# Optimization experiments

Hardware: AMD Instinct MI355X
Metric: run time of the kernel (lower is better)

## Reference

```python
import jax, jax.numpy as jnp
import numpy as np

EPS = 1e-5

def _layernorm(x, gamma, beta):
    mu = jnp.mean(x, axis=-1, keepdims=True)
    var = jnp.mean(jnp.square(x - mu), axis=-1, keepdims=True)
    return (x - mu) * jax.lax.rsqrt(var + EPS) * gamma + beta

def setup_inputs() -> dict:
    key = jax.random.key(0)
    k1, k2, k3 = jax.random.split(key, 3)
    T, B, D, H = 512, 32, 1024, 1024
    s_x = 1.0 / np.sqrt(D)
    s_h = 1.0 / np.sqrt(H)
    return {
        "input": jax.random.normal(k1, (T, B, D), dtype=jnp.float32),
        "h0": jnp.zeros((B, H), dtype=jnp.float32),
        "c0": jnp.zeros((B, H), dtype=jnp.float32),
        "Wx": jax.random.normal(k2, (4 * H, D), dtype=jnp.float32) * s_x,
        "Wh": jax.random.normal(k3, (4 * H, H), dtype=jnp.float32) * s_h,
        "gn_gamma": jnp.ones((4 * H,), dtype=jnp.float32),
        "gn_beta": jnp.zeros((4 * H,), dtype=jnp.float32),
        "cn_gamma": jnp.ones((H,), dtype=jnp.float32),
        "cn_beta": jnp.zeros((H,), dtype=jnp.float32),
    }

def reference(input, h0, c0, Wx, Wh, gn_gamma, gn_beta, cn_gamma, cn_beta):
    H = h0.shape[-1]
    # Precompute input projection for all timesteps: [T, B, 4H]
    gated_input = jnp.einsum('tbd,gd->tbg', input, Wx)

    def step(carry, gates_x):
        h, c = carry
        gates = gates_x + h @ Wh.T            # [B, 4H]
        gates = _layernorm(gates, gn_gamma, gn_beta)
        i, f, g, o = jnp.split(gates, 4, axis=1)
        c = jax.nn.sigmoid(f) * c + jax.nn.sigmoid(i) * jnp.tanh(g)
        c = _layernorm(c, cn_gamma, cn_beta)
        h = jax.nn.sigmoid(o) * jnp.tanh(c)
        return (h, c), h

    (h, c), output = jax.lax.scan(step, (h0, c0), gated_input)
    return output, h, c
```

## Files before the change

kernel.cpp:

```cpp
#include <hip/hip_runtime.h>
#include <hip/hip_bf16.h>

typedef __hip_bfloat16 bf16;
typedef __attribute__((ext_vector_type(4))) float f32x4;
typedef __attribute__((ext_vector_type(8))) short bf16x8;
typedef unsigned long long u64;
typedef unsigned short u16;
typedef unsigned u32;

#define T_STEPS 512
#define BATCH   32
#define DIM     1024
#define HID     1024
#define GATES   4096
#define NPROD   64
#define NOWN    32
#define NSCAN   (NPROD + NOWN)
#define MTILES  128
#define NTILES  16
#define NGEMM   (MTILES * NTILES)
#define MAGIC   0x5EED0001u

static __device__ __forceinline__ float sigmf(float x) {
    return 1.0f / (1.0f + __expf(-x));
}
static __device__ __forceinline__ float tanhfast(float x) {
    return 1.0f - 2.0f / (__expf(2.0f * x) + 1.0f);
}

static __device__ __forceinline__ u64 ldc_u64(const u64* p) {
    return __hip_atomic_load((u64*)p, __ATOMIC_RELAXED, __HIP_MEMORY_SCOPE_AGENT);
}
static __device__ __forceinline__ void stc_u64(u64* p, u64 v) {
    __hip_atomic_store(p, v, __ATOMIC_RELAXED, __HIP_MEMORY_SCOPE_AGENT);
}
static __device__ __forceinline__ void stc_u32(u32* p, u32 v) {
    __hip_atomic_store(p, v, __ATOMIC_RELAXED, __HIP_MEMORY_SCOPE_AGENT);
}
static __device__ __forceinline__ u32 ldc_u32(const u32* p) {
    return __hip_atomic_load((u32*)p, __ATOMIC_RELAXED, __HIP_MEMORY_SCOPE_AGENT);
}

static __device__ __forceinline__ bf16x8 cvt8(const float* p) {
    float4 x = *(const float4*)p;
    float4 y = *(const float4*)(p + 4);
    bf16x8 r;
    ((u16*)&r)[0] = __bfloat16_as_ushort(__float2bfloat16(x.x));
    ((u16*)&r)[1] = __bfloat16_as_ushort(__float2bfloat16(x.y));
    ((u16*)&r)[2] = __bfloat16_as_ushort(__float2bfloat16(x.z));
    ((u16*)&r)[3] = __bfloat16_as_ushort(__float2bfloat16(x.w));
    ((u16*)&r)[4] = __bfloat16_as_ushort(__float2bfloat16(y.x));
    ((u16*)&r)[5] = __bfloat16_as_ushort(__float2bfloat16(y.y));
    ((u16*)&r)[6] = __bfloat16_as_ushort(__float2bfloat16(y.z));
    ((u16*)&r)[7] = __bfloat16_as_ushort(__float2bfloat16(y.w));
    return r;
}

__global__ void init_kernel(u32* __restrict__ hx,
                            u64* __restrict__ gates_u,
                            u32* __restrict__ gxsent) {
    const size_t stride = (size_t)gridDim.x * blockDim.x;
    const size_t t0 = (size_t)blockIdx.x * blockDim.x + threadIdx.x;
    for (size_t i = t0; i < (size_t)BATCH * HID; i += stride) hx[i] = 0xFFFFFFFFu;
    for (size_t i = t0; i < (size_t)BATCH * GATES; i += stride) gates_u[i] = 0;
    for (size_t i = t0; i < (size_t)MTILES * NTILES; i += stride) gxsent[i] = 0u;
}

__global__ __launch_bounds__(512, 2) void fused_kernel(
    const float* __restrict__ input,
    const float* __restrict__ Wx,
    const float* __restrict__ Wh,
    const float* __restrict__ h0,
    const float* __restrict__ c0,
    const float* __restrict__ gn_g, const float* __restrict__ gn_b,
    const float* __restrict__ cn_g, const float* __restrict__ cn_b,
    u32* __restrict__ hx,
    u64* __restrict__ gates_u,
    bf16* __restrict__ gxT,
    u32* __restrict__ gxsent,
    float* __restrict__ out,
    float* __restrict__ h_final,
    float* __restrict__ c_final) {

    const int tid  = threadIdx.x;
    const int lane = tid & 63;
    const int w    = tid >> 6;

    if (blockIdx.x >= NSCAN) {
        const int gid = blockIdx.x - NSCAN;
        const int bm = gid >> 4;
        const int bn = gid & 15;
        const int wm = (w >> 2) * 64, wn = (w & 3) * 64;
        const int lr = lane & 15;
        const int ko = (lane >> 4) * 8;

        const float* Af = input + (size_t)(bm * 128 + wm + lr) * DIM + ko;
        const float* Bf = Wx    + (size_t)(bn * 256 + wn + lr) * DIM + ko;

        f32x4 acc[4][4] = {};
        for (int k = 0; k < DIM; k += 32) {
            bf16x8 af[4], bw[4];
#pragma unroll
            for (int m = 0; m < 4; ++m)
                af[m] = cvt8(Af + (size_t)m * 16 * DIM + k);
#pragma unroll
            for (int n = 0; n < 4; ++n)
                bw[n] = cvt8(Bf + (size_t)n * 16 * DIM + k);
#pragma unroll
            for (int m = 0; m < 4; ++m)
#pragma unroll
                for (int n = 0; n < 4; ++n)
                    acc[m][n] = __builtin_amdgcn_mfma_f32_16x16x32_bf16(af[m], bw[n], acc[m][n], 0, 0, 0);
        }
        const int cr = (lane >> 4) * 4;
        u64* gxT64 = (u64*)gxT;
#pragma unroll
        for (int m = 0; m < 4; ++m)
#pragma unroll
            for (int n = 0; n < 4; ++n) {
                int col = bn * 256 + wn + n * 16 + lr;
                int rb  = bm * 128 + wm + m * 16 + cr;
                u64 pk = 0;
#pragma unroll
                for (int r = 0; r < 4; ++r)
                    pk |= (u64)__bfloat16_as_ushort(__float2bfloat16(acc[m][n][r])) << (16 * r);
                stc_u64(gxT64 + (size_t)col * 4096 + (rb >> 2), pk);
            }
        asm volatile("s_waitcnt vmcnt(0)" ::: "memory");
        __syncthreads();
        if (tid == 0) stc_u32(gxsent + bm * NTILES + bn, MAGIC);
        return;
    }

    if (blockIdx.x < NPROD) {
        const int mi   = blockIdx.x & 1;
        const int g    = blockIdx.x >> 1;
        const int ni   = g * 8 + w;
        const int lr   = lane & 15;
        const int hi   = lane >> 4;
        const int ko   = hi * 8;
        const int cr   = hi * 4;
        const int gcol = ni * 16 + lr;
        const int brow = mi * 16 + cr;

        __shared__ __align__(16) char hsm[16 * 2048];

        const float* wf = Wh + (size_t)gcol * DIM + ko;
        bf16x8 bfrag[32];
#pragma unroll
        for (int kk = 0; kk < 32; ++kk)
            bfrag[kk] = cvt8(wf + kk * 32);

        const int arow = lr * 2048;
        const int axor = (lr & 7) << 4;

        const u64* gxT64 = (const u64*)gxT;
        const int ntile = g >> 1;
        u16 gxu[4];
        {
            int mtile = (2 * 0 + mi) >> 3;
            u32 sv = ldc_u32(gxsent + mtile * NTILES + ntile);
            while (sv != MAGIC) {
                __builtin_amdgcn_s_sleep(2);
                sv = ldc_u32(gxsent + mtile * NTILES + ntile);
            }
            u64 v = ldc_u64(gxT64 + (size_t)gcol * 4096 + 0 * 8 + mi * 4 + hi);
            gxu[0] = (u16)v; gxu[1] = (u16)(v >> 16);
            gxu[2] = (u16)(v >> 32); gxu[3] = (u16)(v >> 48);
        }

        for (int t = 0; t < T_STEPS; ++t) {
            {
                const int row0 = 2 * w + (lane >> 5);
                const int l5 = lane & 31;
                const u64* hsrc = (const u64*)(hx + (size_t)(mi * 16 + row0) * HID);
                char* drow = hsm + row0 * 2048;
                const int sx = (row0 & 7) << 4;
                const u32 want = (u32)t;
                u64 vv[16];
#pragma unroll
                for (int k = 0; k < 16; ++k)
                    vv[k] = ldc_u64(hsrc + k * 32 + l5);
                for (;;) {
                    bool ok = true;
#pragma unroll
                    for (int k = 0; k < 16; ++k) {
                        if ((((u32)(vv[k] >> 16) & 0xFFFFu) != want) ||
                            ((u32)(vv[k] >> 48) != want)) {
                            ok = false;
                            vv[k] = ldc_u64(hsrc + k * 32 + l5);
                        }
                    }
                    if (ok) break;
                    __builtin_amdgcn_s_sleep(1);
                }
#pragma unroll
                for (int k = 0; k < 16; ++k) {
                    int j = k * 32 + l5;
                    u32 packed = (u32)(vv[k] & 0xFFFFu) |
                                 (((u32)(vv[k] >> 32) & 0xFFFFu) << 16);
                    *(u32*)(drow + ((4 * j) ^ sx)) = packed;
                }
            }
            __syncthreads();

            {
                f32x4 acc = {0.f, 0.f, 0.f, 0.f};
#pragma unroll
                for (int kk = 0; kk < 32; ++kk) {
                    bf16x8 a = *(const bf16x8*)(hsm + arow + ((kk * 64 + ko * 2) ^ axor));
                    acc = __builtin_amdgcn_mfma_f32_16x16x32_bf16(a, bfrag[kk], acc, 0, 0, 0);
                }
                u64* gp = gates_u + (size_t)brow * GATES + gcol;
                const u64 tagup = (u64)(u32)(t + 1) << 32;
#pragma unroll
                for (int r = 0; r < 4; ++r) {
                    union { u16 u; bf16 h; } cv; cv.u = gxu[r];
                    float val = acc[r] + __bfloat162float(cv.h);
                    stc_u64(gp + (size_t)r * GATES, tagup | (u64)__float_as_uint(val));
                }
            }

            if (t + 1 < T_STEPS) {
                int tn = t + 1;
                int mtile = (2 * tn + mi) >> 3;
                u32 sv = ldc_u32(gxsent + mtile * NTILES + ntile);
                while (sv != MAGIC) {
                    __builtin_amdgcn_s_sleep(2);
                    sv = ldc_u32(gxsent + mtile * NTILES + ntile);
                }
                u64 v = ldc_u64(gxT64 + (size_t)gcol * 4096 + tn * 8 + mi * 4 + hi);
                gxu[0] = (u16)v; gxu[1] = (u16)(v >> 16);
                gxu[2] = (u16)(v >> 32); gxu[3] = (u16)(v >> 48);
            }
        }
        return;
    }

    const int b = blockIdx.x - NPROD;
    __shared__ float red[2][8];

    float creg[2];
#pragma unroll
    for (int q = 0; q < 2; ++q) creg[q] = c0[b * HID + 2 * tid + q];

    {
        u32 e0 = (u32)__bfloat16_as_ushort(__float2bfloat16(h0[b * HID + 2 * tid]));
        u32 e1 = (u32)__bfloat16_as_ushort(__float2bfloat16(h0[b * HID + 2 * tid + 1]));
        stc_u64((u64*)(hx + (size_t)b * HID + 2 * tid), (u64)e0 | ((u64)e1 << 32));
    }

    for (int t = 0; t < T_STEPS; ++t) {
        const u64* grow = gates_u + (size_t)b * GATES;
        const u32 want = (u32)(t + 1);
        u64 vg[4][2];
#pragma unroll
        for (int q = 0; q < 4; ++q)
#pragma unroll
            for (int e = 0; e < 2; ++e)
                vg[q][e] = ldc_u64(grow + q * 1024 + 2 * tid + e);
        for (;;) {
            bool ok = true;
#pragma unroll
            for (int q = 0; q < 4; ++q)
#pragma unroll
                for (int e = 0; e < 2; ++e)
                    if ((u32)(vg[q][e] >> 32) != want) {
                        ok = false;
                        vg[q][e] = ldc_u64(grow + q * 1024 + 2 * tid + e);
                    }
            if (ok) break;
            __builtin_amdgcn_s_sleep(1);
        }
        float gv[4][2];
        float s = 0.f, s2 = 0.f;
#pragma unroll
        for (int q = 0; q < 4; ++q)
#pragma unroll
            for (int e = 0; e < 2; ++e) {
                float x = __uint_as_float((u32)vg[q][e]);
                gv[q][e] = x;
                s += x; s2 += x * x;
            }
#pragma unroll
        for (int off = 32; off > 0; off >>= 1) {
            s  += __shfl_down(s, off, 64);
            s2 += __shfl_down(s2, off, 64);
        }
        if (lane == 0) { red[0][w] = s; red[1][w] = s2; }
        __syncthreads();
        s  = red[0][0] + red[0][1] + red[0][2] + red[0][3]
           + red[0][4] + red[0][5] + red[0][6] + red[0][7];
        s2 = red[1][0] + red[1][1] + red[1][2] + red[1][3]
           + red[1][4] + red[1][5] + red[1][6] + red[1][7];
        const float mu   = s * (1.0f / GATES);
        const float rstd = rsqrtf(s2 * (1.0f / GATES) - mu * mu + 1e-5f);

        float ov[2], cn_[2];
        float cs = 0.f, cs2 = 0.f;
#pragma unroll
        for (int q = 0; q < 2; ++q) {
            int j = 2 * tid + q;
            float iv = sigmf(   (gv[0][q] - mu) * rstd * gn_g[j]           + gn_b[j]);
            float fv = sigmf(   (gv[1][q] - mu) * rstd * gn_g[HID + j]     + gn_b[HID + j]);
            float gg = tanhfast((gv[2][q] - mu) * rstd * gn_g[2 * HID + j] + gn_b[2 * HID + j]);
            ov[q] =             (gv[3][q] - mu) * rstd * gn_g[3 * HID + j] + gn_b[3 * HID + j];
            float cnew = fv * creg[q] + iv * gg;
            cn_[q] = cnew;
            cs += cnew; cs2 += cnew * cnew;
        }
#pragma unroll
        for (int off = 32; off > 0; off >>= 1) {
            cs  += __shfl_down(cs, off, 64);
            cs2 += __shfl_down(cs2, off, 64);
        }
        __syncthreads();
        if (lane == 0) { red[0][w] = cs; red[1][w] = cs2; }
        __syncthreads();
        cs  = red[0][0] + red[0][1] + red[0][2] + red[0][3]
            + red[0][4] + red[0][5] + red[0][6] + red[0][7];
        cs2 = red[1][0] + red[1][1] + red[1][2] + red[1][3]
            + red[1][4] + red[1][5] + red[1][6] + red[1][7];
        const float mu2   = cs * (1.0f / HID);
        const float rstd2 = rsqrtf(cs2 * (1.0f / HID) - mu2 * mu2 + 1e-5f);

        float hv_[2];
        u32 he[2];
#pragma unroll
        for (int q = 0; q < 2; ++q) {
            float cn = (cn_[q] - mu2) * rstd2 * cn_g[2 * tid + q] + cn_b[2 * tid + q];
            creg[q] = cn;
            hv_[q] = sigmf(ov[q]) * tanhfast(cn);
            he[q] = ((u32)(t + 1) << 16) |
                    (u32)__bfloat16_as_ushort(__float2bfloat16(hv_[q]));
        }
        stc_u64((u64*)(hx + (size_t)b * HID + 2 * tid),
                (u64)he[0] | ((u64)he[1] << 32));

        float* orow = out + ((size_t)t * BATCH + b) * HID + 2 * tid;
#pragma unroll
        for (int q = 0; q < 2; ++q)
            __builtin_nontemporal_store(hv_[q], orow + q);
        if (t == T_STEPS - 1) {
#pragma unroll
            for (int q = 0; q < 2; ++q) {
                h_final[b * HID + 2 * tid + q] = hv_[q];
                c_final[b * HID + 2 * tid + q] = creg[q];
            }
        }
    }
}

extern "C" void kernel_launch(void* const* d_in, const int* in_sizes, int n_in,
                              void* d_out, int out_size, void* d_ws, size_t ws_size,
                              hipStream_t stream) {
    const float* input = (const float*)d_in[0];
    const float* h0    = (const float*)d_in[1];
    const float* c0    = (const float*)d_in[2];
    const float* Wx    = (const float*)d_in[3];
    const float* Wh    = (const float*)d_in[4];
    const float* gn_g  = (const float*)d_in[5];
    const float* gn_b  = (const float*)d_in[6];
    const float* cn_g  = (const float*)d_in[7];
    const float* cn_b  = (const float*)d_in[8];

    char* ws = (char*)d_ws;
    size_t off = 0;
    auto alloc = [&](size_t bytes) -> char* {
        char* p = ws + off;
        off += (bytes + 255) & ~(size_t)255;
        return p;
    };
    u64*  gates_u = (u64*) alloc((size_t)BATCH * GATES * 8);
    u32*  hx      = (u32*) alloc((size_t)BATCH * HID * 4);
    u32*  gxsent  = (u32*) alloc((size_t)MTILES * NTILES * 4);
    bf16* gxT     = (bf16*)alloc((size_t)GATES * (T_STEPS * BATCH) * 2);

    float* outp    = (float*)d_out;
    float* h_final = outp + (size_t)T_STEPS * BATCH * HID;
    float* c_final = h_final + (size_t)BATCH * HID;

    hipLaunchKernelGGL(init_kernel, dim3(256), dim3(256), 0, stream,
                       hx, gates_u, gxsent);

    hipLaunchKernelGGL(fused_kernel, dim3(NSCAN + NGEMM), dim3(512), 0, stream,
                       input, Wx, Wh, h0, c0, gn_g, gn_b, cn_g, cn_b,
                       hx, gates_u, gxT, gxsent, outp, h_final, c_final);
}
```

Measured before the change: 3.818 ms.

## Split recurrent GEMM producers into four batch domains and drop one LN barrier

The recurrent h@Wh^T producers are repartitioned from 2 batch halves to 4 batch domains of 8 rows, doubling the producer block count to 128 and placing owner blocks first in the grid. Each producer now polls and stages only 8 h rows per step, which cuts per-block spin traffic and LDS use but leaves half the MFMA rows as duplicates whose results are discarded. Owner blocks use a separate shared buffer for the cell-state layernorm reduction so one __syncthreads per step can be removed. The trade is more blocks contending for the GPU's CUs and wasted MFMA work, in exchange for shorter per-step critical paths.

```diff
diff --git a/kernel.cpp b/kernel.cpp
--- a/kernel.cpp
+++ b/kernel.cpp
@@ -13,9 +13,10 @@
 #define DIM     1024
 #define HID     1024
 #define GATES   4096
-#define NPROD   64
+#define NDOM    4
 #define NOWN    32
-#define NSCAN   (NPROD + NOWN)
+#define NPROD   128
+#define NSCAN   (NOWN + NPROD)
 #define MTILES  128
 #define NTILES  16
 #define NGEMM   (MTILES * NTILES)
@@ -132,18 +133,17 @@
         return;
     }
 
-    if (blockIdx.x < NPROD) {
-        const int mi   = blockIdx.x & 1;
-        const int g    = blockIdx.x >> 1;
+    if (blockIdx.x >= NOWN) {
+        const int pid  = blockIdx.x - NOWN;
+        const int d    = pid & 3;
+        const int g    = pid >> 2;
         const int ni   = g * 8 + w;
         const int lr   = lane & 15;
         const int hi   = lane >> 4;
         const int ko   = hi * 8;
-        const int cr   = hi * 4;
         const int gcol = ni * 16 + lr;
-        const int brow = mi * 16 + cr;
-
-        __shared__ __align__(16) char hsm[16 * 2048];
+
+        __shared__ __align__(16) char hsm[8 * 2048];
 
         const float* wf = Wh + (size_t)gcol * DIM + ko;
         bf16x8 bfrag[32];
@@ -151,52 +151,49 @@
         for (int kk = 0; kk < 32; ++kk)
             bfrag[kk] = cvt8(wf + kk * 32);
 
-        const int arow = lr * 2048;
+        const int arow = (lr & 7) * 2048;
         const int axor = (lr & 7) << 4;
 
         const u64* gxT64 = (const u64*)gxT;
         const int ntile = g >> 1;
         u16 gxu[4];
         {
-            int mtile = (2 * 0 + mi) >> 3;
-            u32 sv = ldc_u32(gxsent + mtile * NTILES + ntile);
+            u32 sv = ldc_u32(gxsent + 0 * NTILES + ntile);
             while (sv != MAGIC) {
                 __builtin_amdgcn_s_sleep(2);
-                sv = ldc_u32(gxsent + mtile * NTILES + ntile);
-            }
-            u64 v = ldc_u64(gxT64 + (size_t)gcol * 4096 + 0 * 8 + mi * 4 + hi);
+                sv = ldc_u32(gxsent + 0 * NTILES + ntile);
+            }
+            u64 v = ldc_u64(gxT64 + (size_t)gcol * 4096 + 2 * d + (hi & 1));
             gxu[0] = (u16)v; gxu[1] = (u16)(v >> 16);
             gxu[2] = (u16)(v >> 32); gxu[3] = (u16)(v >> 48);
         }
 
         for (int t = 0; t < T_STEPS; ++t) {
             {
-                const int row0 = 2 * w + (lane >> 5);
-                const int l5 = lane & 31;
-                const u64* hsrc = (const u64*)(hx + (size_t)(mi * 16 + row0) * HID);
-                char* drow = hsm + row0 * 2048;
-                const int sx = (row0 & 7) << 4;
+                const u64* hsrc = (const u64*)(hx + (size_t)(8 * d + w) * HID);
+                char* drow = hsm + w * 2048;
+                const int sx = w << 4;
                 const u32 want = (u32)t;
-                u64 vv[16];
-#pragma unroll
-                for (int k = 0; k < 16; ++k)
-                    vv[k] = ldc_u64(hsrc + k * 32 + l5);
+                u64 vv[8];
+#pragma unroll
+                for (int k = 0; k < 8; ++k)
+                    vv[k] = ldc_u64(hsrc + k * 64 + lane);
                 for (;;) {
                     bool ok = true;
 #pragma unroll
-                    for (int k = 0; k < 16; ++k) {
+                    for (int k = 0; k < 8; ++k) {
                         if ((((u32)(vv[k] >> 16) & 0xFFFFu) != want) ||
                             ((u32)(vv[k] >> 48) != want)) {
                             ok = false;
-                            vv[k] = ldc_u64(hsrc + k * 32 + l5);
+                            vv[k] = ldc_u64(hsrc + k * 64 + lane);
                         }
                     }
                     if (ok) break;
                     __builtin_amdgcn_s_sleep(1);
                 }
 #pragma unroll
-                for (int k = 0; k < 16; ++k) {
-                    int j = k * 32 + l5;
+                for (int k = 0; k < 8; ++k) {
+                    int j = k * 64 + lane;
                     u32 packed = (u32)(vv[k] & 0xFFFFu) |
                                  (((u32)(vv[k] >> 32) & 0xFFFFu) << 16);
                     *(u32*)(drow + ((4 * j) ^ sx)) = packed;
@@ -211,25 +208,27 @@
                     bf16x8 a = *(const bf16x8*)(hsm + arow + ((kk * 64 + ko * 2) ^ axor));
                     acc = __builtin_amdgcn_mfma_f32_16x16x32_bf16(a, bfrag[kk], acc, 0, 0, 0);
                 }
-                u64* gp = gates_u + (size_t)brow * GATES + gcol;
-                const u64 tagup = (u64)(u32)(t + 1) << 32;
-#pragma unroll
-                for (int r = 0; r < 4; ++r) {
-                    union { u16 u; bf16 h; } cv; cv.u = gxu[r];
-                    float val = acc[r] + __bfloat162float(cv.h);
-                    stc_u64(gp + (size_t)r * GATES, tagup | (u64)__float_as_uint(val));
+                if (hi < 2) {
+                    u64* gp = gates_u + (size_t)(8 * d + hi * 4) * GATES + gcol;
+                    const u64 tagup = (u64)(u32)(t + 1) << 32;
+#pragma unroll
+                    for (int r = 0; r < 4; ++r) {
+                        union { u16 u; bf16 h; } cv; cv.u = gxu[r];
+                        float val = acc[r] + __bfloat162float(cv.h);
+                        stc_u64(gp + (size_t)r * GATES, tagup | (u64)__float_as_uint(val));
+                    }
                 }
             }
 
             if (t + 1 < T_STEPS) {
                 int tn = t + 1;
-                int mtile = (2 * tn + mi) >> 3;
+                int mtile = (4 * tn + d) >> 4;
                 u32 sv = ldc_u32(gxsent + mtile * NTILES + ntile);
                 while (sv != MAGIC) {
                     __builtin_amdgcn_s_sleep(2);
                     sv = ldc_u32(gxsent + mtile * NTILES + ntile);
                 }
-                u64 v = ldc_u64(gxT64 + (size_t)gcol * 4096 + tn * 8 + mi * 4 + hi);
+                u64 v = ldc_u64(gxT64 + (size_t)gcol * 4096 + tn * 8 + 2 * d + (hi & 1));
                 gxu[0] = (u16)v; gxu[1] = (u16)(v >> 16);
                 gxu[2] = (u16)(v >> 32); gxu[3] = (u16)(v >> 48);
             }
@@ -237,8 +236,9 @@
         return;
     }
 
-    const int b = blockIdx.x - NPROD;
+    const int b = blockIdx.x;
     __shared__ float red[2][8];
+    __shared__ float redc[2][8];
 
     float creg[2];
 #pragma unroll
@@ -264,11 +264,11 @@
 #pragma unroll
             for (int q = 0; q < 4; ++q)
 #pragma unroll
-                for (int e = 0; e < 2; ++e)
-                    if ((u32)(vg[q][e] >> 32) != want) {
-                        ok = false;
-                        vg[q][e] = ldc_u64(grow + q * 1024 + 2 * tid + e);
-                    }
+            for (int e = 0; e < 2; ++e)
+                if ((u32)(vg[q][e] >> 32) != want) {
+                    ok = false;
+                    vg[q][e] = ldc_u64(grow + q * 1024 + 2 * tid + e);
+                }
             if (ok) break;
             __builtin_amdgcn_s_sleep(1);
         }
@@ -314,13 +314,12 @@
             cs  += __shfl_down(cs, off, 64);
             cs2 += __shfl_down(cs2, off, 64);
         }
+        if (lane == 0) { redc[0][w] = cs; redc[1][w] = cs2; }
         __syncthreads();
-        if (lane == 0) { red[0][w] = cs; red[1][w] = cs2; }
-        __syncthreads();
-        cs  = red[0][0] + red[0][1] + red[0][2] + red[0][3]
-            + red[0][4] + red[0][5] + red[0][6] + red[0][7];
-        cs2 = red[1][0] + red[1][1] + red[1][2] + red[1][3]
-            + red[1][4] + red[1][5] + red[1][6] + red[1][7];
+        cs  = redc[0][0] + redc[0][1] + redc[0][2] + redc[0][3]
+            + redc[0][4] + redc[0][5] + redc[0][6] + redc[0][7];
+        cs2 = redc[1][0] + redc[1][1] + redc[1][2] + redc[1][3]
+            + redc[1][4] + redc[1][5] + redc[1][6] + redc[1][7];
         const float mu2   = cs * (1.0f / HID);
         const float rstd2 = rsqrtf(cs2 * (1.0f / HID) - mu2 * mu2 + 1e-5f);
 
```

Measured after the change: 3.350 ms. 12.3% less time.
